# Optimization experiments

Measured on AMD Instinct MI355X. Metric: run time of the kernel, lower is better.

Reference implementation:

```python
import jax, jax.numpy as jnp
import numpy as np

N, E, D, H, C = 50000, 1600000, 256, 8, 32

def setup_inputs() -> dict:
    key = jax.random.key(0)
    ks = jax.random.split(key, 7)
    feat = jax.random.normal(ks[0], (N, D), dtype=jnp.float32)
    edge_weight = jax.random.uniform(ks[1], (E,), dtype=jnp.float32)
    W_lin = jax.random.normal(ks[2], (D, H * C), dtype=jnp.float32) * (1.0 / np.sqrt(D))
    att_l = jax.random.normal(ks[3], (1, H, C), dtype=jnp.float32) * (1.0 / np.sqrt(H))
    att_r = jax.random.normal(ks[4], (1, H, C), dtype=jnp.float32) * (1.0 / np.sqrt(H))
    W_res = jax.random.normal(ks[5], (D, H * C), dtype=jnp.float32) * (1.0 / np.sqrt(D))
    edge_index = jax.random.randint(ks[6], (2, E), 0, N, dtype=jnp.int32)
    return {"feat": feat, "edge_weight": edge_weight, "W_lin": W_lin,
            "att_l": att_l, "att_r": att_r, "W_res": W_res, "edge_index": edge_index}

def reference(feat, edge_weight, W_lin, att_l, att_r, W_res, edge_index):
    n_nodes = feat.shape[0]
    h, c = att_l.shape[1], att_l.shape[2]
    src, dst = edge_index[0], edge_index[1]
    # node projection: [N, H, C]
    x = (feat @ W_lin).reshape(n_nodes, h, c)
    alpha_l = (x * att_l).sum(-1)  # [N, H]
    alpha_r = (x * att_r).sum(-1)  # [N, H]
    # per-edge scores [E, H]
    alpha = alpha_l[src] + alpha_r[dst]
    alpha = edge_weight[:, None] * alpha
    alpha = jnp.where(alpha > 0, alpha, 0.2 * alpha)  # leaky_relu(0.2)
    # segment softmax over destination nodes
    amax = jax.lax.stop_gradient(jax.ops.segment_max(alpha, dst, num_segments=n_nodes))
    ex = jnp.exp(alpha - amax[dst])
    denom = jax.ops.segment_sum(ex, dst, num_segments=n_nodes)
    coeff = ex / (denom[dst] + 1e-16)  # [E, H]
    # weighted message aggregation
    msg = x[src] * coeff[:, :, None]  # [E, H, C]
    agg = jax.ops.segment_sum(msg, dst, num_segments=n_nodes)  # [N, H, C]
    out = jax.nn.elu(agg).reshape(n_nodes, h * c)
    out = out + feat @ W_res  # residual
    return out
```

## Files before the change

kernel.cpp:

```cpp
#include <hip/hip_runtime.h>
#include <stdint.h>

#define D_DIM 256
#define NPAD  640

typedef __bf16 bf16x8 __attribute__((ext_vector_type(8)));
typedef float  f32x4  __attribute__((ext_vector_type(4)));

__device__ __forceinline__ float bf2f(unsigned short u) {
  union { unsigned int i; float f; } cv; cv.i = ((unsigned int)u) << 16; return cv.f;
}
__device__ __forceinline__ unsigned short f2bf(float f) {
  union { float f; unsigned int i; } cv; cv.f = f;
  unsigned int i = cv.i;
  unsigned int lsb = (i >> 16) & 1u;
  i += 0x7fffu + lsb;
  return (unsigned short)(i >> 16);
}
__device__ __forceinline__ void gld16(const void* gptr, void* lptr) {
  __builtin_amdgcn_global_load_lds(
      (const __attribute__((address_space(1))) unsigned int*)gptr,
      (__attribute__((address_space(3))) unsigned int*)lptr, 16, 0, 0);
}

__global__ __launch_bounds__(256) void setup_cvt_prep(
    const float* __restrict__ feat, unsigned short* __restrict__ fb,
    const float* __restrict__ W_lin, const float* __restrict__ W_res,
    const float* __restrict__ att_l, const float* __restrict__ att_r,
    unsigned short* __restrict__ Bt, int nelem, int nb_cvt) {
  int bid = blockIdx.x, t = threadIdx.x;
  if (bid < nb_cvt) {
    int i = (bid * 256 + t) * 8;
    if (i >= nelem) return;
    float4 v0 = *(const float4*)(feat + i);
    float4 v1 = *(const float4*)(feat + i + 4);
    ushort4 a, b;
    a.x = f2bf(v0.x); a.y = f2bf(v0.y); a.z = f2bf(v0.z); a.w = f2bf(v0.w);
    b.x = f2bf(v1.x); b.y = f2bf(v1.y); b.z = f2bf(v1.z); b.w = f2bf(v1.w);
    *(ushort4*)(fb + i) = a;
    *(ushort4*)(fb + i + 4) = b;
  } else {
    int idx = (bid - nb_cvt) * 256 + t;
    int n = idx >> 8, k = idx & 255;
    float v = 0.f;
    if (n < 256) v = W_lin[k * 256 + n];
    else if (n < 512) v = W_res[k * 256 + (n - 256)];
    else if (n < 520) {
      int h = n - 512; float s = 0.f;
      #pragma unroll
      for (int c = 0; c < 32; ++c) s += W_lin[k * 256 + h * 32 + c] * att_l[h * 32 + c];
      v = s;
    } else if (n < 528) {
      int h = n - 520; float s = 0.f;
      #pragma unroll
      for (int c = 0; c < 32; ++c) s += W_lin[k * 256 + h * 32 + c] * att_r[h * 32 + c];
      v = s;
    }
    Bt[idx] = f2bf(v);
  }
}

__global__ __launch_bounds__(256) void scan_partial(const int* __restrict__ cnt,
                                                    int* __restrict__ bsum, int N) {
  __shared__ int s[256];
  int t = threadIdx.x;
  int i = blockIdx.x * 256 + t;
  s[t] = (i < N) ? cnt[i] : 0;
  __syncthreads();
  for (int off = 128; off > 0; off >>= 1) {
    if (t < off) s[t] += s[t + off];
    __syncthreads();
  }
  if (t == 0) bsum[blockIdx.x] = s[0];
}

__global__ __launch_bounds__(256) void scan_top(int* __restrict__ bsum, int nb) {
  __shared__ int s[256];
  int t = threadIdx.x;
  int v = (t < nb) ? bsum[t] : 0;
  s[t] = v;
  __syncthreads();
  for (int off = 1; off < 256; off <<= 1) {
    int u = (t >= off) ? s[t - off] : 0;
    __syncthreads();
    s[t] += u;
    __syncthreads();
  }
  if (t < nb) bsum[t] = s[t] - v;
}

__global__ __launch_bounds__(256) void scan_apply(const int* __restrict__ cnt,
                                                  const int* __restrict__ bsum,
                                                  int* __restrict__ row_ptr, int N) {
  __shared__ int s[256];
  int t = threadIdx.x;
  int i = blockIdx.x * 256 + t;
  int v = (i < N) ? cnt[i] : 0;
  s[t] = v;
  __syncthreads();
  for (int off = 1; off < 256; off <<= 1) {
    int u = (t >= off) ? s[t - off] : 0;
    __syncthreads();
    s[t] += u;
    __syncthreads();
  }
  int excl = bsum[blockIdx.x] + s[t] - v;
  if (i < N) {
    row_ptr[i] = excl;
    if (i == N - 1) row_ptr[N] = excl + v;
  }
}

__global__ __launch_bounds__(256) void gemm_hist(
    const unsigned short* __restrict__ A,
    const unsigned short* __restrict__ Bt,
    float* __restrict__ out, unsigned short* __restrict__ xbf,
    float* __restrict__ alpha_l, float* __restrict__ alpha_r, int M,
    const int* __restrict__ dst, int* __restrict__ cnt, int* __restrict__ rank,
    int E, int nb_hist, int gx) {
  __shared__ unsigned short As[128 * 32];
  __shared__ unsigned short Bs[128 * 32];

  if ((int)blockIdx.x < nb_hist) {
    int base = (int)blockIdx.x * 2048 + threadIdx.x;
    #pragma unroll
    for (int u = 0; u < 8; ++u) {
      int e = base + u * 256;
      if (e < E) rank[e] = atomicAdd(&cnt[dst[e]], 1);
    }
    return;
  }

  int tid  = threadIdx.x;
  int w    = tid >> 6, lane = tid & 63;
  int gb   = (int)blockIdx.x - nb_hist;
  int bm   = (gb % gx) * 128, bn = (gb / gx) * 128;
  int wm   = (w & 1) * 64, wn = (w >> 1) * 64;
  int l16  = lane & 15, quad = lane >> 4;

  f32x4 acc[4][4] = {};

  int srow = w * 32 + (lane >> 2);
  int koff = (lane & 3) * 8;

  for (int k0 = 0; k0 < 256; k0 += 32) {
    #pragma unroll
    for (int i = 0; i < 2; ++i) {
      int r  = srow + i * 16;
      int rg = bm + r; if (rg > M - 1) rg = M - 1;
      gld16(A  + (size_t)rg * 256 + k0 + koff, &As[(w * 32 + i * 16) * 32]);
      gld16(Bt + (size_t)(bn + r) * 256 + k0 + koff, &Bs[(w * 32 + i * 16) * 32]);
    }
    __syncthreads();
    bf16x8 a[4], b[4];
    #pragma unroll
    for (int mi = 0; mi < 4; ++mi)
      a[mi] = *(const bf16x8*)&As[(wm + mi * 16 + l16) * 32 + quad * 8];
    #pragma unroll
    for (int ni = 0; ni < 4; ++ni)
      b[ni] = *(const bf16x8*)&Bs[(wn + ni * 16 + l16) * 32 + quad * 8];
    #pragma unroll
    for (int mi = 0; mi < 4; ++mi)
      #pragma unroll
      for (int ni = 0; ni < 4; ++ni)
        acc[mi][ni] = __builtin_amdgcn_mfma_f32_16x16x32_bf16(a[mi], b[ni], acc[mi][ni], 0, 0, 0);
    __syncthreads();
  }

  #pragma unroll
  for (int mi = 0; mi < 4; ++mi) {
    #pragma unroll
    for (int r = 0; r < 4; ++r) {
      int row = bm + wm + mi * 16 + quad * 4 + r;
      if (row >= M) continue;
      #pragma unroll
      for (int ni = 0; ni < 4; ++ni) {
        int n = bn + wn + ni * 16 + l16;
        float v = acc[mi][ni][r];
        if (n < 256)      xbf[(size_t)row * 256 + n] = f2bf(v);
        else if (n < 512) out[(size_t)row * 256 + (n - 256)] = v;
        else if (n < 520) alpha_l[row * 8 + (n - 512)] = v;
        else if (n < 528) alpha_r[row * 8 + (n - 520)] = v;
      }
    }
  }
}

__global__ __launch_bounds__(256) void scatter_kernel(
    const int* __restrict__ eidx, const float* __restrict__ ew,
    const int* __restrict__ row_ptr, const int* __restrict__ rank,
    int2* __restrict__ pairs, int E) {
  int e = blockIdx.x * 256 + threadIdx.x;
  if (e < E) {
    int d = eidx[E + e];
    int pos = row_ptr[d] + rank[e];
    int2 p; p.x = eidx[e]; p.y = __float_as_int(ew[e]);
    pairs[pos] = p;
  }
}

__global__ __launch_bounds__(256) void agg_kernel(
    const int* __restrict__ row_ptr, const int2* __restrict__ pairs,
    const float* __restrict__ alpha_l, const float* __restrict__ alpha_r,
    const unsigned short* __restrict__ xbf, float* __restrict__ out, int N) {
  int node = blockIdx.x * 4 + (threadIdx.x >> 6);
  if (node >= N) return;
  int lane = threadIdx.x & 63;
  int h  = lane >> 3;
  int cb = lane << 2;

  int beg = row_ptr[node], end = row_ptr[node + 1];
  float arv = alpha_r[node * 8 + h];
  float l = 0.f;
  float ac0 = 0.f, ac1 = 0.f, ac2 = 0.f, ac3 = 0.f;

  if (beg < end) {
    int last = end - 1;
    const unsigned short* xb = xbf + cb;
    for (int jg = beg; jg < end; jg += 4) {
      int2 q[4];
      #pragma unroll
      for (int u = 0; u < 4; ++u) {
        int t = jg + u; t = (t < last) ? t : last;
        q[u] = pairs[t];
      }
      float al[4];
      #pragma unroll
      for (int u = 0; u < 4; ++u) al[u] = alpha_l[(size_t)q[u].x * 8 + h];
      ushort4 xv[4];
      #pragma unroll
      for (int u = 0; u < 4; ++u)
        xv[u] = *(const ushort4*)(xb + ((size_t)q[u].x << 8));
      #pragma unroll
      for (int u = 0; u < 4; ++u) {
        float a = __int_as_float(q[u].y) * (al[u] + arv);
        a = (a > 0.f) ? a : 0.2f * a;
        float p = __expf(a);
        p = (jg + u < end) ? p : 0.f;
        l += p;
        ac0 = fmaf(p, bf2f(xv[u].x), ac0);
        ac1 = fmaf(p, bf2f(xv[u].y), ac1);
        ac2 = fmaf(p, bf2f(xv[u].z), ac2);
        ac3 = fmaf(p, bf2f(xv[u].w), ac3);
      }
    }
  }
  float r = 1.0f / (l + 1e-16f);
  float o0 = ac0 * r, o1 = ac1 * r, o2 = ac2 * r, o3 = ac3 * r;
  o0 = (o0 > 0.f) ? o0 : expm1f(o0);
  o1 = (o1 > 0.f) ? o1 : expm1f(o1);
  o2 = (o2 > 0.f) ? o2 : expm1f(o2);
  o3 = (o3 > 0.f) ? o3 : expm1f(o3);
  float4* op = (float4*)(out + ((size_t)node << 8) + cb);
  float4 res = *op;
  res.x += o0; res.y += o1; res.z += o2; res.w += o3;
  *op = res;
}

extern "C" void kernel_launch(void* const* d_in, const int* in_sizes, int n_in,
                              void* d_out, int out_size, void* d_ws, size_t ws_size,
                              hipStream_t stream) {
  const float* feat  = (const float*)d_in[0];
  const float* ew    = (const float*)d_in[1];
  const float* W_lin = (const float*)d_in[2];
  const float* att_l = (const float*)d_in[3];
  const float* att_r = (const float*)d_in[4];
  const float* W_res = (const float*)d_in[5];
  const int*   eidx  = (const int*)d_in[6];
  float* out = (float*)d_out;

  int N = in_sizes[0] / D_DIM;
  int E = in_sizes[1];

  char* p = (char*)d_ws;
  auto alloc = [&](size_t bytes) {
    char* r = p; p += (bytes + 255) & ~(size_t)255; return r;
  };
  unsigned short* xbf  = (unsigned short*)alloc((size_t)N * 256 * 2);
  unsigned short* fb   = (unsigned short*)alloc((size_t)N * 256 * 2);
  float* alpha_l       = (float*)alloc((size_t)N * 8 * 4);
  float* alpha_r       = (float*)alloc((size_t)N * 8 * 4);
  unsigned short* Bt   = (unsigned short*)alloc((size_t)NPAD * D_DIM * 2);
  int*   row_ptr       = (int*)alloc((size_t)(N + 1) * 4);
  int*   cnt           = (int*)alloc((size_t)N * 4);
  int*   rank          = (int*)alloc((size_t)E * 4);
  int*   bsum          = (int*)alloc(1024);
  int2*  pairs_sep     = (int2*)alloc((size_t)E * 8);
  bool sep_ok = ((size_t)((char*)(pairs_sep + E) - (char*)d_ws) <= ws_size);
  int2* pairs = sep_ok ? pairs_sep : (int2*)fb;

  int nb      = (N + 255) / 256;
  int nb_cvt  = (N * 256 / 8 + 255) / 256;
  int nb_prep = NPAD * D_DIM / 256;
  int nb_hist = (E + 2047) / 2048;
  int nb_scat = (E + 255) / 256;
  int gx = (N + 127) / 128;
  int gemm_blocks = gx * (NPAD / 128);

  hipMemsetAsync(cnt, 0, (size_t)N * 4, stream);

  setup_cvt_prep<<<nb_cvt + nb_prep, 256, 0, stream>>>(
      feat, fb, W_lin, W_res, att_l, att_r, Bt, N * 256, nb_cvt);

  gemm_hist<<<nb_hist + gemm_blocks, 256, 0, stream>>>(
      fb, Bt, out, xbf, alpha_l, alpha_r, N,
      eidx + E, cnt, rank, E, nb_hist, gx);

  scan_partial<<<nb, 256, 0, stream>>>(cnt, bsum, N);
  scan_top<<<1, 256, 0, stream>>>(bsum, nb);
  scan_apply<<<nb, 256, 0, stream>>>(cnt, bsum, row_ptr, N);

  scatter_kernel<<<nb_scat, 256, 0, stream>>>(eidx, ew, row_ptr, rank, pairs, E);

  agg_kernel<<<(N + 3) / 4, 256, 0, stream>>>(row_ptr, pairs, alpha_l, alpha_r, xbf, out, N);
}
```

Measured before the change: 415.2 us.

## Precompute per-edge exp scores in scatter and split node aggregation across two waves

Moves the per-edge attention score computation (alpha gather, leaky relu, exp) from the aggregation kernel into the scatter kernel, which stores bf16 exp values per edge per head alongside a separate source-index array. The exp is now computed once per edge and head instead of once per lane, which removes redundant alpha_l gathers in aggregation. Aggregation assigns two wavefronts per node that each take alternate groups of four edges, then combines the partial sums through shared memory, adding parallelism for high-degree nodes. In exchange, the unnormalized exp weights are rounded to bf16, the scatter kernel writes more bytes, and each block needs a barrier.

```diff
diff --git a/kernel.cpp b/kernel.cpp
--- a/kernel.cpp
+++ b/kernel.cpp
@@ -189,72 +189,100 @@
 __global__ __launch_bounds__(256) void scatter_kernel(
     const int* __restrict__ eidx, const float* __restrict__ ew,
     const int* __restrict__ row_ptr, const int* __restrict__ rank,
-    int2* __restrict__ pairs, int E) {
+    const float* __restrict__ alpha_l, const float* __restrict__ alpha_r,
+    int* __restrict__ srcA, unsigned short* __restrict__ pexp, int E) {
   int e = blockIdx.x * 256 + threadIdx.x;
-  if (e < E) {
-    int d = eidx[E + e];
-    int pos = row_ptr[d] + rank[e];
-    int2 p; p.x = eidx[e]; p.y = __float_as_int(ew[e]);
-    pairs[pos] = p;
-  }
+  if (e >= E) return;
+  int s = eidx[e], d = eidx[E + e];
+  int pos = row_ptr[d] + rank[e];
+  float w = ew[e];
+  float4 al0 = *(const float4*)(alpha_l + (size_t)s * 8);
+  float4 al1 = *(const float4*)(alpha_l + (size_t)s * 8 + 4);
+  float4 ar0 = *(const float4*)(alpha_r + (size_t)d * 8);
+  float4 ar1 = *(const float4*)(alpha_r + (size_t)d * 8 + 4);
+  float a[8] = {al0.x + ar0.x, al0.y + ar0.y, al0.z + ar0.z, al0.w + ar0.w,
+                al1.x + ar1.x, al1.y + ar1.y, al1.z + ar1.z, al1.w + ar1.w};
+  ushort4 o0, o1;
+  unsigned short pb[8];
+  #pragma unroll
+  for (int h = 0; h < 8; ++h) {
+    float v = w * a[h];
+    v = (v > 0.f) ? v : 0.2f * v;
+    pb[h] = f2bf(__expf(v));
+  }
+  o0.x = pb[0]; o0.y = pb[1]; o0.z = pb[2]; o0.w = pb[3];
+  o1.x = pb[4]; o1.y = pb[5]; o1.z = pb[6]; o1.w = pb[7];
+  srcA[pos] = s;
+  *(ushort4*)(pexp + (size_t)pos * 8) = o0;
+  *(ushort4*)(pexp + (size_t)pos * 8 + 4) = o1;
 }
 
 __global__ __launch_bounds__(256) void agg_kernel(
-    const int* __restrict__ row_ptr, const int2* __restrict__ pairs,
-    const float* __restrict__ alpha_l, const float* __restrict__ alpha_r,
+    const int* __restrict__ row_ptr, const int* __restrict__ srcA,
+    const unsigned short* __restrict__ pexp,
     const unsigned short* __restrict__ xbf, float* __restrict__ out, int N) {
-  int node = blockIdx.x * 4 + (threadIdx.x >> 6);
-  if (node >= N) return;
+  __shared__ float red[2][64][6];
+  int nin  = threadIdx.x >> 7;
+  int wv   = (threadIdx.x >> 6) & 1;
   int lane = threadIdx.x & 63;
+  int node = blockIdx.x * 2 + nin;
+  bool active = node < N;
   int h  = lane >> 3;
   int cb = lane << 2;
 
-  int beg = row_ptr[node], end = row_ptr[node + 1];
-  float arv = alpha_r[node * 8 + h];
-  float l = 0.f;
-  float ac0 = 0.f, ac1 = 0.f, ac2 = 0.f, ac3 = 0.f;
-
-  if (beg < end) {
-    int last = end - 1;
-    const unsigned short* xb = xbf + cb;
-    for (int jg = beg; jg < end; jg += 4) {
-      int2 q[4];
-      #pragma unroll
-      for (int u = 0; u < 4; ++u) {
-        int t = jg + u; t = (t < last) ? t : last;
-        q[u] = pairs[t];
+  float l = 0.f, ac0 = 0.f, ac1 = 0.f, ac2 = 0.f, ac3 = 0.f;
+
+  if (active) {
+    int beg = row_ptr[node], end = row_ptr[node + 1];
+    if (beg < end) {
+      int last = end - 1;
+      const unsigned short* xb = xbf + cb;
+      for (int jg = beg + wv * 4; jg < end; jg += 8) {
+        int s[4]; float pv[4];
+        #pragma unroll
+        for (int u = 0; u < 4; ++u) {
+          int t = jg + u; t = (t < last) ? t : last;
+          s[u]  = srcA[t];
+          pv[u] = bf2f(pexp[(size_t)t * 8 + h]);
+        }
+        ushort4 xv[4];
+        #pragma unroll
+        for (int u = 0; u < 4; ++u)
+          xv[u] = *(const ushort4*)(xb + ((size_t)s[u] << 8));
+        #pragma unroll
+        for (int u = 0; u < 4; ++u) {
+          float p = (jg + u < end) ? pv[u] : 0.f;
+          l += p;
+          ac0 = fmaf(p, bf2f(xv[u].x), ac0);
+          ac1 = fmaf(p, bf2f(xv[u].y), ac1);
+          ac2 = fmaf(p, bf2f(xv[u].z), ac2);
+          ac3 = fmaf(p, bf2f(xv[u].w), ac3);
+        }
       }
-      float al[4];
-      #pragma unroll
-      for (int u = 0; u < 4; ++u) al[u] = alpha_l[(size_t)q[u].x * 8 + h];
-      ushort4 xv[4];
-      #pragma unroll
-      for (int u = 0; u < 4; ++u)
-        xv[u] = *(const ushort4*)(xb + ((size_t)q[u].x << 8));
-      #pragma unroll
-      for (int u = 0; u < 4; ++u) {
-        float a = __int_as_float(q[u].y) * (al[u] + arv);
-        a = (a > 0.f) ? a : 0.2f * a;
-        float p = __expf(a);
-        p = (jg + u < end) ? p : 0.f;
-        l += p;
-        ac0 = fmaf(p, bf2f(xv[u].x), ac0);
-        ac1 = fmaf(p, bf2f(xv[u].y), ac1);
-        ac2 = fmaf(p, bf2f(xv[u].z), ac2);
-        ac3 = fmaf(p, bf2f(xv[u].w), ac3);
-      }
-    }
-  }
-  float r = 1.0f / (l + 1e-16f);
-  float o0 = ac0 * r, o1 = ac1 * r, o2 = ac2 * r, o3 = ac3 * r;
-  o0 = (o0 > 0.f) ? o0 : expm1f(o0);
-  o1 = (o1 > 0.f) ? o1 : expm1f(o1);
-  o2 = (o2 > 0.f) ? o2 : expm1f(o2);
-  o3 = (o3 > 0.f) ? o3 : expm1f(o3);
-  float4* op = (float4*)(out + ((size_t)node << 8) + cb);
-  float4 res = *op;
-  res.x += o0; res.y += o1; res.z += o2; res.w += o3;
-  *op = res;
+    }
+  }
+
+  if (wv == 1) {
+    red[nin][lane][0] = l;
+    red[nin][lane][1] = ac0; red[nin][lane][2] = ac1;
+    red[nin][lane][3] = ac2; red[nin][lane][4] = ac3;
+  }
+  __syncthreads();
+  if (active && wv == 0) {
+    l   += red[nin][lane][0];
+    ac0 += red[nin][lane][1]; ac1 += red[nin][lane][2];
+    ac2 += red[nin][lane][3]; ac3 += red[nin][lane][4];
+    float r = 1.0f / (l + 1e-16f);
+    float o0 = ac0 * r, o1 = ac1 * r, o2 = ac2 * r, o3 = ac3 * r;
+    o0 = (o0 > 0.f) ? o0 : expm1f(o0);
+    o1 = (o1 > 0.f) ? o1 : expm1f(o1);
+    o2 = (o2 > 0.f) ? o2 : expm1f(o2);
+    o3 = (o3 > 0.f) ? o3 : expm1f(o3);
+    float4* op = (float4*)(out + ((size_t)node << 8) + cb);
+    float4 res = *op;
+    res.x += o0; res.y += o1; res.z += o2; res.w += o3;
+    *op = res;
+  }
 }
 
 extern "C" void kernel_launch(void* const* d_in, const int* in_sizes, int n_in,
@@ -285,9 +313,10 @@
   int*   cnt           = (int*)alloc((size_t)N * 4);
   int*   rank          = (int*)alloc((size_t)E * 4);
   int*   bsum          = (int*)alloc(1024);
-  int2*  pairs_sep     = (int2*)alloc((size_t)E * 8);
-  bool sep_ok = ((size_t)((char*)(pairs_sep + E) - (char*)d_ws) <= ws_size);
-  int2* pairs = sep_ok ? pairs_sep : (int2*)fb;
+  int*   srcA          = (int*)alloc((size_t)E * 4);
+  unsigned short* pexp_sep = (unsigned short*)alloc((size_t)E * 8 * 2);
+  bool sep_ok = ((size_t)((char*)(pexp_sep + (size_t)E * 8) - (char*)d_ws) <= ws_size);
+  unsigned short* pexp = sep_ok ? pexp_sep : fb;
 
   int nb      = (N + 255) / 256;
   int nb_cvt  = (N * 256 / 8 + 255) / 256;
@@ -310,7 +339,8 @@
   scan_top<<<1, 256, 0, stream>>>(bsum, nb);
   scan_apply<<<nb, 256, 0, stream>>>(cnt, bsum, row_ptr, N);
 
-  scatter_kernel<<<nb_scat, 256, 0, stream>>>(eidx, ew, row_ptr, rank, pairs, E);
-
-  agg_kernel<<<(N + 3) / 4, 256, 0, stream>>>(row_ptr, pairs, alpha_l, alpha_r, xbf, out, N);
-}
+  scatter_kernel<<<nb_scat, 256, 0, stream>>>(
+      eidx, ew, row_ptr, rank, alpha_l, alpha_r, srcA, pexp, E);
+
+  agg_kernel<<<(N + 1) / 2, 256, 0, stream>>>(row_ptr, srcA, pexp, xbf, out, N);
+}
```

Result: slower. 457.8 us (+10.3%).

## Split node aggregation across two waves and widen GEMM K-tile with swizzled LDS

Applied to the files above, without the earlier changes.

The aggregation kernel now gives each destination node two wavefronts. They take interleaved groups of 4 edges and combine their partial softmax sums and accumulators through shared memory, which doubles the memory-level parallelism for the gather-heavy edge loop. Separately, the GEMM loads a 64-wide K slab per iteration into an XOR-swizzled LDS layout, halving the number of barriers and avoiding bank conflicts on fragment reads. The costs are an extra block-wide sync and LDS reduction per node, twice the LDS usage in the GEMM, and more blocks in the aggregation launch.

```diff
diff --git a/kernel.cpp b/kernel.cpp
--- a/kernel.cpp
+++ b/kernel.cpp
@@ -118,8 +118,8 @@
     float* __restrict__ alpha_l, float* __restrict__ alpha_r, int M,
     const int* __restrict__ dst, int* __restrict__ cnt, int* __restrict__ rank,
     int E, int nb_hist, int gx) {
-  __shared__ unsigned short As[128 * 32];
-  __shared__ unsigned short Bs[128 * 32];
+  __shared__ unsigned short As[128 * 64];
+  __shared__ unsigned short Bs[128 * 64];
 
   if ((int)blockIdx.x < nb_hist) {
     int base = (int)blockIdx.x * 2048 + threadIdx.x;
@@ -140,30 +140,39 @@
 
   f32x4 acc[4][4] = {};
 
-  int srow = w * 32 + (lane >> 2);
-  int koff = (lane & 3) * 8;
-
-  for (int k0 = 0; k0 < 256; k0 += 32) {
+  int sr8     = lane >> 3;
+  int koff_sw = (((lane & 7) ^ sr8) * 8);
+
+  for (int k0 = 0; k0 < 256; k0 += 64) {
     #pragma unroll
-    for (int i = 0; i < 2; ++i) {
-      int r  = srow + i * 16;
-      int rg = bm + r; if (rg > M - 1) rg = M - 1;
-      gld16(A  + (size_t)rg * 256 + k0 + koff, &As[(w * 32 + i * 16) * 32]);
-      gld16(Bt + (size_t)(bn + r) * 256 + k0 + koff, &Bs[(w * 32 + i * 16) * 32]);
-    }
-    __syncthreads();
-    bf16x8 a[4], b[4];
+    for (int j = 0; j < 4; ++j) {
+      int rbase = w * 32 + j * 8;
+      int rga = bm + rbase + sr8; if (rga > M - 1) rga = M - 1;
+      gld16(A  + (size_t)rga * 256 + k0 + koff_sw, &As[rbase * 64]);
+      gld16(Bt + (size_t)(bn + rbase + sr8) * 256 + k0 + koff_sw, &Bs[rbase * 64]);
+    }
+    __syncthreads();
     #pragma unroll
-    for (int mi = 0; mi < 4; ++mi)
-      a[mi] = *(const bf16x8*)&As[(wm + mi * 16 + l16) * 32 + quad * 8];
-    #pragma unroll
-    for (int ni = 0; ni < 4; ++ni)
-      b[ni] = *(const bf16x8*)&Bs[(wn + ni * 16 + l16) * 32 + quad * 8];
-    #pragma unroll
-    for (int mi = 0; mi < 4; ++mi)
-      #pragma unroll
-      for (int ni = 0; ni < 4; ++ni)
-        acc[mi][ni] = __builtin_amdgcn_mfma_f32_16x16x32_bf16(a[mi], b[ni], acc[mi][ni], 0, 0, 0);
+    for (int kk = 0; kk < 64; kk += 32) {
+      bf16x8 a[4], b[4];
+      #pragma unroll
+      for (int mi = 0; mi < 4; ++mi) {
+        int r = wm + mi * 16 + l16;
+        int col = (kk * 2 + quad * 16) ^ ((r & 7) << 4);
+        a[mi] = *(const bf16x8*)((const char*)&As[r * 64] + col);
+      }
+      #pragma unroll
+      for (int ni = 0; ni < 4; ++ni) {
+        int r = wn + ni * 16 + l16;
+        int col = (kk * 2 + quad * 16) ^ ((r & 7) << 4);
+        b[ni] = *(const bf16x8*)((const char*)&Bs[r * 64] + col);
+      }
+      #pragma unroll
+      for (int mi = 0; mi < 4; ++mi)
+        #pragma unroll
+        for (int ni = 0; ni < 4; ++ni)
+          acc[mi][ni] = __builtin_amdgcn_mfma_f32_16x16x32_bf16(a[mi], b[ni], acc[mi][ni], 0, 0, 0);
+    }
     __syncthreads();
   }
 
@@ -203,58 +212,74 @@
     const int* __restrict__ row_ptr, const int2* __restrict__ pairs,
     const float* __restrict__ alpha_l, const float* __restrict__ alpha_r,
     const unsigned short* __restrict__ xbf, float* __restrict__ out, int N) {
-  int node = blockIdx.x * 4 + (threadIdx.x >> 6);
-  if (node >= N) return;
+  __shared__ float red[2][64][6];
+  int nin  = threadIdx.x >> 7;
+  int wv   = (threadIdx.x >> 6) & 1;
   int lane = threadIdx.x & 63;
+  int node = blockIdx.x * 2 + nin;
+  bool active = node < N;
   int h  = lane >> 3;
   int cb = lane << 2;
 
-  int beg = row_ptr[node], end = row_ptr[node + 1];
-  float arv = alpha_r[node * 8 + h];
-  float l = 0.f;
-  float ac0 = 0.f, ac1 = 0.f, ac2 = 0.f, ac3 = 0.f;
-
-  if (beg < end) {
-    int last = end - 1;
-    const unsigned short* xb = xbf + cb;
-    for (int jg = beg; jg < end; jg += 4) {
-      int2 q[4];
-      #pragma unroll
-      for (int u = 0; u < 4; ++u) {
-        int t = jg + u; t = (t < last) ? t : last;
-        q[u] = pairs[t];
+  float l = 0.f, ac0 = 0.f, ac1 = 0.f, ac2 = 0.f, ac3 = 0.f;
+
+  if (active) {
+    int beg = row_ptr[node], end = row_ptr[node + 1];
+    if (beg < end) {
+      float arv = alpha_r[node * 8 + h];
+      int last = end - 1;
+      const unsigned short* xb = xbf + cb;
+      for (int jg = beg + wv * 4; jg < end; jg += 8) {
+        int2 q[4];
+        #pragma unroll
+        for (int u = 0; u < 4; ++u) {
+          int t = jg + u; t = (t < last) ? t : last;
+          q[u] = pairs[t];
+        }
+        float al[4];
+        #pragma unroll
+        for (int u = 0; u < 4; ++u) al[u] = alpha_l[(size_t)q[u].x * 8 + h];
+        ushort4 xv[4];
+        #pragma unroll
+        for (int u = 0; u < 4; ++u)
+          xv[u] = *(const ushort4*)(xb + ((size_t)q[u].x << 8));
+        #pragma unroll
+        for (int u = 0; u < 4; ++u) {
+          float a = __int_as_float(q[u].y) * (al[u] + arv);
+          a = (a > 0.f) ? a : 0.2f * a;
+          float p = __expf(a);
+          p = (jg + u < end) ? p : 0.f;
+          l += p;
+          ac0 = fmaf(p, bf2f(xv[u].x), ac0);
+          ac1 = fmaf(p, bf2f(xv[u].y), ac1);
+          ac2 = fmaf(p, bf2f(xv[u].z), ac2);
+          ac3 = fmaf(p, bf2f(xv[u].w), ac3);
+        }
       }
-      float al[4];
-      #pragma unroll
-      for (int u = 0; u < 4; ++u) al[u] = alpha_l[(size_t)q[u].x * 8 + h];
-      ushort4 xv[4];
-      #pragma unroll
-      for (int u = 0; u < 4; ++u)
-        xv[u] = *(const ushort4*)(xb + ((size_t)q[u].x << 8));
-      #pragma unroll
-      for (int u = 0; u < 4; ++u) {
-        float a = __int_as_float(q[u].y) * (al[u] + arv);
-        a = (a > 0.f) ? a : 0.2f * a;
-        float p = __expf(a);
-        p = (jg + u < end) ? p : 0.f;
-        l += p;
-        ac0 = fmaf(p, bf2f(xv[u].x), ac0);
-        ac1 = fmaf(p, bf2f(xv[u].y), ac1);
-        ac2 = fmaf(p, bf2f(xv[u].z), ac2);
-        ac3 = fmaf(p, bf2f(xv[u].w), ac3);
-      }
-    }
-  }
-  float r = 1.0f / (l + 1e-16f);
-  float o0 = ac0 * r, o1 = ac1 * r, o2 = ac2 * r, o3 = ac3 * r;
-  o0 = (o0 > 0.f) ? o0 : expm1f(o0);
-  o1 = (o1 > 0.f) ? o1 : expm1f(o1);
-  o2 = (o2 > 0.f) ? o2 : expm1f(o2);
-  o3 = (o3 > 0.f) ? o3 : expm1f(o3);
-  float4* op = (float4*)(out + ((size_t)node << 8) + cb);
-  float4 res = *op;
-  res.x += o0; res.y += o1; res.z += o2; res.w += o3;
-  *op = res;
+    }
+  }
+
+  if (wv == 1) {
+    red[nin][lane][0] = l;
+    red[nin][lane][1] = ac0; red[nin][lane][2] = ac1;
+    red[nin][lane][3] = ac2; red[nin][lane][4] = ac3;
+  }
+  __syncthreads();
+  if (active && wv == 0) {
+    l   += red[nin][lane][0];
+    ac0 += red[nin][lane][1]; ac1 += red[nin][lane][2];
+    ac2 += red[nin][lane][3]; ac3 += red[nin][lane][4];
+    float r = 1.0f / (l + 1e-16f);
+    float o0 = ac0 * r, o1 = ac1 * r, o2 = ac2 * r, o3 = ac3 * r;
+    o0 = (o0 > 0.f) ? o0 : expm1f(o0);
+    o1 = (o1 > 0.f) ? o1 : expm1f(o1);
+    o2 = (o2 > 0.f) ? o2 : expm1f(o2);
+    o3 = (o3 > 0.f) ? o3 : expm1f(o3);
+    float4* op = (float4*)(out + ((size_t)node << 8) + cb);
+    float4 res = *op;
+    res.x += o0; res.y += o1; res.z += o2; res.w += o3;
+    *op = res;
+  }
 }
 
 extern "C" void kernel_launch(void* const* d_in, const int* in_sizes, int n_in,
@@ -312,5 +337,5 @@
 
   scatter_kernel<<<nb_scat, 256, 0, stream>>>(eidx, ew, row_ptr, rank, pairs, E);
 
-  agg_kernel<<<(N + 3) / 4, 256, 0, stream>>>(row_ptr, pairs, alpha_l, alpha_r, xbf, out, N);
-}
+  agg_kernel<<<(N + 1) / 2, 256, 0, stream>>>(row_ptr, pairs, alpha_l, alpha_r, xbf, out, N);
+}
```

Measured after the change: 408.7 us. No clear change (-1.6%).
